# Kernel optimization log

Measured on AMD Instinct MI355X. Metric: run time of the kernel, lower is better.

The kernel has to match this reference:

```python
import jax, jax.numpy as jnp
import numpy as np

N = 100_000      # nodes
E = 1_600_000    # edges (avg degree 16)
D = 64           # node feature dim
C = 2            # num_classes
K = 2            # propagation hops


def setup_inputs() -> dict:
    key = jax.random.key(0)
    k1, k2, k3 = jax.random.split(key, 3)
    x = jax.random.normal(k1, (N, D), dtype=jnp.float32)
    edge_index = jax.random.randint(k2, (2, E), 0, N, dtype=jnp.int64)
    W = jax.random.normal(k3, (C, D), dtype=jnp.float32) * 0.1  # torch Linear weight [out,in]
    b = jnp.zeros((C,), dtype=jnp.float32)
    return {"x": x, "edge_index": edge_index, "W": W, "b": b}


def reference(x, edge_index, W, b):
    n = x.shape[0]
    self_loop = jnp.arange(n, dtype=edge_index.dtype)
    row = jnp.concatenate([edge_index[0], self_loop])  # source
    col = jnp.concatenate([edge_index[1], self_loop])  # target
    # GCN symmetric normalization with self-loops (PyG gcn_norm)
    deg = jax.ops.segment_sum(jnp.ones(col.shape, dtype=x.dtype), col, num_segments=n)
    dinv = jnp.where(deg > 0, jax.lax.rsqrt(deg), 0.0)
    norm = dinv[row] * dinv[col]                      # [E+N]
    # K-hop propagation: x <- A_hat x
    for _ in range(K):
        x = jax.ops.segment_sum(norm[:, None] * x[row], col, num_segments=n)
    logits = x @ W.T + b                               # [N, C]
    return jax.nn.log_softmax(logits, axis=1)
```

## Files before the change

kernel.cpp:

```cpp
#include <hip/hip_runtime.h>
#include <hip/hip_bf16.h>
#include <math.h>


#define NODES 100000
#define EDGES 1600000
#define DIM 64

#define PBITS 8
#define PSIZE 256
#define P_BUCKETS 391
#define CAP 8192

#define PART_BLOCKS 128
#define PART_PAIRS (EDGES / 2 / PART_BLOCKS)

#define PROJ_BLOCKS 782
#define NODES_PER_PROJ 128
#define K1_BLOCKS (PART_BLOCKS + PROJ_BLOCKS)

__global__ __launch_bounds__(256) void partproj_kernel(
    const void* __restrict__ ei, int* __restrict__ cursor,
    int* __restrict__ ecbuf, const float* __restrict__ x,
    const float* __restrict__ W, float4* __restrict__ uq) {
  const int t = threadIdx.x;
  if (blockIdx.x < PART_BLOCKS) {
    __shared__ int shMode;
    __shared__ int lcnt[P_BUCKETS];
    __shared__ int lbase[P_BUCKETS];
    if (t < 64) {
      const int* p = (const int*)ei;
      unsigned long long ball = __ballot(p[2 * t + 1] == 0);
      if (t == 0) shMode = (ball == ~0ULL) ? 1 : 0;
    }
    for (int i = t; i < P_BUCKETS; i += 256) lcnt[i] = 0;
    __syncthreads();
    const int m = shMode;
    const int pbase = blockIdx.x * PART_PAIRS;

    if (m) {
      const longlong2* cp =
          (const longlong2*)((const long long*)ei + EDGES) + pbase;
      for (int i = t; i < PART_PAIRS; i += 256) {
        longlong2 v = cp[i];
        atomicAdd(&lcnt[((int)v.x) >> PBITS], 1);
        atomicAdd(&lcnt[((int)v.y) >> PBITS], 1);
      }
    } else {
      const int2* cp = (const int2*)((const int*)ei + EDGES) + pbase;
      for (int i = t; i < PART_PAIRS; i += 256) {
        int2 v = cp[i];
        atomicAdd(&lcnt[v.x >> PBITS], 1);
        atomicAdd(&lcnt[v.y >> PBITS], 1);
      }
    }
    __syncthreads();
    for (int i = t; i < P_BUCKETS; i += 256) {
      int c = lcnt[i];
      lbase[i] = c ? atomicAdd(&cursor[i], c) : 0;
      lcnt[i] = 0;
    }
    __syncthreads();

    if (m) {
      const longlong2* rp = (const longlong2*)ei + pbase;
      const longlong2* cp =
          (const longlong2*)((const long long*)ei + EDGES) + pbase;
      for (int i = t; i < PART_PAIRS; i += 256) {
        longlong2 rv = rp[i];
        longlong2 cv = cp[i];
        {
          int r = (int)rv.x, c = (int)cv.x, bk = c >> PBITS;
          int rel = lbase[bk] + atomicAdd(&lcnt[bk], 1);
          if (rel < CAP)
            ecbuf[bk * CAP + rel] = (r << PBITS) | (c & (PSIZE - 1));
        }
        {
          int r = (int)rv.y, c = (int)cv.y, bk = c >> PBITS;
          int rel = lbase[bk] + atomicAdd(&lcnt[bk], 1);
          if (rel < CAP)
            ecbuf[bk * CAP + rel] = (r << PBITS) | (c & (PSIZE - 1));
        }
      }
    } else {
      const int2* rp = (const int2*)ei + pbase;
      const int2* cp = (const int2*)((const int*)ei + EDGES) + pbase;
      for (int i = t; i < PART_PAIRS; i += 256) {
        int2 rv = rp[i];
        int2 cv = cp[i];
        {
          int bk = cv.x >> PBITS;
          int rel = lbase[bk] + atomicAdd(&lcnt[bk], 1);
          if (rel < CAP)
            ecbuf[bk * CAP + rel] = (rv.x << PBITS) | (cv.x & (PSIZE - 1));
        }
        {
          int bk = cv.y >> PBITS;
          int rel = lbase[bk] + atomicAdd(&lcnt[bk], 1);
          if (rel < CAP)
            ecbuf[bk * CAP + rel] = (rv.y << PBITS) | (cv.y & (PSIZE - 1));
        }
      }
    }
  } else {
    const int nbase = (blockIdx.x - PART_BLOCKS) * NODES_PER_PROJ;
    const int lane16 = t & 15;
    const int sub = t >> 4;
    const float4 w0 = *(const float4*)&W[lane16 * 4];
    const float4 w1 = *(const float4*)&W[DIM + lane16 * 4];
    for (int k = sub; k < NODES_PER_PROJ; k += 16) {
      const int node = nbase + k;
      if (node < NODES) {
        float4 xv = *(const float4*)&x[(size_t)node * DIM + lane16 * 4];
        float p0 = xv.x * w0.x + xv.y * w0.y + xv.z * w0.z + xv.w * w0.w;
        float p1 = xv.x * w1.x + xv.y * w1.y + xv.z * w1.z + xv.w * w1.w;
#pragma unroll
        for (int off = 8; off >= 1; off >>= 1) {
          p0 += __shfl_xor(p0, off, 16);
          p1 += __shfl_xor(p1, off, 16);
        }
        if (lane16 == 0) *(float2*)&uq[node] = make_float2(p0, p1);
      }
    }
  }
}

__global__ __launch_bounds__(1024) void deg_kernel(
    const int* __restrict__ cursor, const int* __restrict__ ecbuf,
    float4* __restrict__ uq) {
  __shared__ int h[PSIZE];
  const int b = blockIdx.x;
  const int t = threadIdx.x;
  if (t < PSIZE) h[t] = 0;
  __syncthreads();
  const int cnt = min(cursor[b], CAP);
  const int4* ep4 = (const int4*)(ecbuf + b * CAP);
  for (int i = t; 4 * i < cnt; i += 1024) {
    int4 v = ep4[i];
    int base = 4 * i;
    if (base + 0 < cnt) atomicAdd(&h[v.x & (PSIZE - 1)], 1);
    if (base + 1 < cnt) atomicAdd(&h[v.y & (PSIZE - 1)], 1);
    if (base + 2 < cnt) atomicAdd(&h[v.z & (PSIZE - 1)], 1);
    if (base + 3 < cnt) atomicAdd(&h[v.w & (PSIZE - 1)], 1);
  }
  __syncthreads();
  if (t < PSIZE) {
    const int node = (b << PBITS) + t;
    if (node < NODES) uq[node].z = rsqrtf((float)(h[t] + 1));
  }
}

__global__ __launch_bounds__(1024) void hop1_kernel(
    const int* __restrict__ cursor, const int* __restrict__ ecbuf,
    const float4* __restrict__ uq, float2* __restrict__ z) {
  __shared__ float ax[PSIZE];
  __shared__ float ay[PSIZE];
  const int b = blockIdx.x;
  const int t = threadIdx.x;
  if (t < PSIZE) {
    ax[t] = 0.f;
    ay[t] = 0.f;
  }
  __syncthreads();
  const int cnt = min(cursor[b], CAP);
  const int4* ep4 = (const int4*)(ecbuf + b * CAP);
  for (int i = t; 4 * i < cnt; i += 1024) {
    int4 v = ep4[i];
    int base = 4 * i;
#pragma unroll
    for (int k = 0; k < 4; k++) {
      int pk = (k == 0) ? v.x : (k == 1) ? v.y : (k == 2) ? v.z : v.w;
      if (base + k < cnt) {
        float4 q = uq[pk >> PBITS];
        int l = pk & (PSIZE - 1);
        atomicAdd(&ax[l], q.z * q.x);
        atomicAdd(&ay[l], q.z * q.y);
      }
    }
  }
  __syncthreads();
  if (t < PSIZE) {
    const int node = (b << PBITS) + t;
    if (node < NODES) {
      float4 q = uq[node];
      float d = q.z;
      float s = d * d;
      z[node] = make_float2(s * (ax[t] + d * q.x), s * (ay[t] + d * q.y));
    }
  }
}

__global__ __launch_bounds__(1024) void hop2_kernel(
    const int* __restrict__ cursor, const int* __restrict__ ecbuf,
    const float2* __restrict__ z, const float4* __restrict__ uq,
    const float* __restrict__ bias, float2* __restrict__ out) {
  __shared__ float ax[PSIZE];
  __shared__ float ay[PSIZE];
  const int b = blockIdx.x;
  const int t = threadIdx.x;
  if (t < PSIZE) {
    ax[t] = 0.f;
    ay[t] = 0.f;
  }
  __syncthreads();
  const int cnt = min(cursor[b], CAP);
  const int4* ep4 = (const int4*)(ecbuf + b * CAP);
  for (int i = t; 4 * i < cnt; i += 1024) {
    int4 v = ep4[i];
    int base = 4 * i;
#pragma unroll
    for (int k = 0; k < 4; k++) {
      int pk = (k == 0) ? v.x : (k == 1) ? v.y : (k == 2) ? v.z : v.w;
      if (base + k < cnt) {
        float2 zv = z[pk >> PBITS];
        int l = pk & (PSIZE - 1);
        atomicAdd(&ax[l], zv.x);
        atomicAdd(&ay[l], zv.y);
      }
    }
  }
  __syncthreads();
  if (t < PSIZE) {
    const int node = (b << PBITS) + t;
    if (node < NODES) {
      float d = uq[node].z;
      float2 zi = z[node];
      float l0 = d * (ax[t] + zi.x) + bias[0];
      float l1 = d * (ay[t] + zi.y) + bias[1];
      float m = fmaxf(l0, l1);
      float ls = m + logf(expf(l0 - m) + expf(l1 - m));
      out[node] = make_float2(l0 - ls, l1 - ls);
    }
  }
}

extern "C" void kernel_launch(void* const* d_in, const int* in_sizes, int n_in,
                              void* d_out, int out_size, void* d_ws,
                              size_t ws_size, hipStream_t stream) {
  const float* x = (const float*)d_in[0];
  const void* ei = d_in[1];
  const float* W = (const float*)d_in[2];
  const float* bias = (const float*)d_in[3];
  float2* out = (float2*)d_out;

  char* w = (char*)d_ws;
  size_t off = 0;
  auto alloc = [&](size_t bytes) -> char* {
    char* p = w + off;
    off += (bytes + 255) & ~(size_t)255;
    return p;
  };
  int* cursor = (int*)alloc(P_BUCKETS * sizeof(int));
  int* ecbuf = (int*)alloc((size_t)P_BUCKETS * CAP * sizeof(int));
  float4* uq = (float4*)alloc((size_t)(P_BUCKETS << PBITS) * sizeof(float4));
  float2* z = (float2*)alloc((size_t)NODES * sizeof(float2));
  (void)ws_size;

  hipMemsetAsync(cursor, 0, P_BUCKETS * sizeof(int), stream);
  partproj_kernel<<<K1_BLOCKS, 256, 0, stream>>>(ei, cursor, ecbuf, x, W, uq);
  deg_kernel<<<P_BUCKETS, 1024, 0, stream>>>(cursor, ecbuf, uq);
  hop1_kernel<<<P_BUCKETS, 1024, 0, stream>>>(cursor, ecbuf, uq, z);
  hop2_kernel<<<P_BUCKETS, 1024, 0, stream>>>(cursor, ecbuf, z, uq, bias, out);
}
```

Before: 159.5 us.

## Halve bucket size, retune partition blocks, and split node data into packed arrays

Shrinks node buckets from 256 to 128 nodes, so there are 782 buckets each handled by a 256-thread block, and raises the partition grid to 625 blocks of 512 threads. It also replaces the float4 per-node record with separate float2 and float arrays. The degree kernel now precomputes d*u, so hop1 gathers 8 bytes per edge instead of 16. The goal is more parallel blocks, smaller per-block working sets, and less gather traffic, at the cost of more global cursor atomics, a tighter CAP margin per bucket (3072 for about 2048 expected edges), and extra writes in the degree kernel.

Measured after the change: 165.8 us. 3.9% more time.

```diff
diff --git a/kernel.cpp b/kernel.cpp
--- a/kernel.cpp
+++ b/kernel.cpp
@@ -7,22 +7,22 @@
 #define EDGES 1600000
 #define DIM 64
 
-#define PBITS 8
-#define PSIZE 256
-#define P_BUCKETS 391
-#define CAP 8192
-
-#define PART_BLOCKS 128
+#define PBITS 7
+#define PSIZE 128
+#define P_BUCKETS 782
+#define CAP 3072
+
+#define PART_BLOCKS 625
 #define PART_PAIRS (EDGES / 2 / PART_BLOCKS)
 
 #define PROJ_BLOCKS 782
 #define NODES_PER_PROJ 128
 #define K1_BLOCKS (PART_BLOCKS + PROJ_BLOCKS)
 
-__global__ __launch_bounds__(256) void partproj_kernel(
+__global__ __launch_bounds__(512) void partproj_kernel(
     const void* __restrict__ ei, int* __restrict__ cursor,
     int* __restrict__ ecbuf, const float* __restrict__ x,
-    const float* __restrict__ W, float4* __restrict__ uq) {
+    const float* __restrict__ W, float2* __restrict__ u) {
   const int t = threadIdx.x;
   if (blockIdx.x < PART_BLOCKS) {
     __shared__ int shMode;
@@ -33,7 +33,7 @@
       unsigned long long ball = __ballot(p[2 * t + 1] == 0);
       if (t == 0) shMode = (ball == ~0ULL) ? 1 : 0;
     }
-    for (int i = t; i < P_BUCKETS; i += 256) lcnt[i] = 0;
+    for (int i = t; i < P_BUCKETS; i += 512) lcnt[i] = 0;
     __syncthreads();
     const int m = shMode;
     const int pbase = blockIdx.x * PART_PAIRS;
@@ -41,21 +41,21 @@
     if (m) {
       const longlong2* cp =
           (const longlong2*)((const long long*)ei + EDGES) + pbase;
-      for (int i = t; i < PART_PAIRS; i += 256) {
+      for (int i = t; i < PART_PAIRS; i += 512) {
         longlong2 v = cp[i];
         atomicAdd(&lcnt[((int)v.x) >> PBITS], 1);
         atomicAdd(&lcnt[((int)v.y) >> PBITS], 1);
       }
     } else {
       const int2* cp = (const int2*)((const int*)ei + EDGES) + pbase;
-      for (int i = t; i < PART_PAIRS; i += 256) {
+      for (int i = t; i < PART_PAIRS; i += 512) {
         int2 v = cp[i];
         atomicAdd(&lcnt[v.x >> PBITS], 1);
         atomicAdd(&lcnt[v.y >> PBITS], 1);
       }
     }
     __syncthreads();
-    for (int i = t; i < P_BUCKETS; i += 256) {
+    for (int i = t; i < P_BUCKETS; i += 512) {
       int c = lcnt[i];
       lbase[i] = c ? atomicAdd(&cursor[i], c) : 0;
       lcnt[i] = 0;
@@ -66,7 +66,7 @@
       const longlong2* rp = (const longlong2*)ei + pbase;
       const longlong2* cp =
           (const longlong2*)((const long long*)ei + EDGES) + pbase;
-      for (int i = t; i < PART_PAIRS; i += 256) {
+      for (int i = t; i < PART_PAIRS; i += 512) {
         longlong2 rv = rp[i];
         longlong2 cv = cp[i];
         {
@@ -85,7 +85,7 @@
     } else {
       const int2* rp = (const int2*)ei + pbase;
       const int2* cp = (const int2*)((const int*)ei + EDGES) + pbase;
-      for (int i = t; i < PART_PAIRS; i += 256) {
+      for (int i = t; i < PART_PAIRS; i += 512) {
         int2 rv = rp[i];
         int2 cv = cp[i];
         {
@@ -108,7 +108,7 @@
     const int sub = t >> 4;
     const float4 w0 = *(const float4*)&W[lane16 * 4];
     const float4 w1 = *(const float4*)&W[DIM + lane16 * 4];
-    for (int k = sub; k < NODES_PER_PROJ; k += 16) {
+    for (int k = sub; k < NODES_PER_PROJ; k += 32) {
       const int node = nbase + k;
       if (node < NODES) {
         float4 xv = *(const float4*)&x[(size_t)node * DIM + lane16 * 4];
@@ -119,15 +119,16 @@
           p0 += __shfl_xor(p0, off, 16);
           p1 += __shfl_xor(p1, off, 16);
         }
-        if (lane16 == 0) *(float2*)&uq[node] = make_float2(p0, p1);
-      }
-    }
-  }
-}
-
-__global__ __launch_bounds__(1024) void deg_kernel(
+        if (lane16 == 0) u[node] = make_float2(p0, p1);
+      }
+    }
+  }
+}
+
+__global__ __launch_bounds__(256) void deg_kernel(
     const int* __restrict__ cursor, const int* __restrict__ ecbuf,
-    float4* __restrict__ uq) {
+    const float2* __restrict__ u, float2* __restrict__ v2,
+    float* __restrict__ dv) {
   __shared__ int h[PSIZE];
   const int b = blockIdx.x;
   const int t = threadIdx.x;
@@ -135,7 +136,7 @@
   __syncthreads();
   const int cnt = min(cursor[b], CAP);
   const int4* ep4 = (const int4*)(ecbuf + b * CAP);
-  for (int i = t; 4 * i < cnt; i += 1024) {
+  for (int i = t; 4 * i < cnt; i += 256) {
     int4 v = ep4[i];
     int base = 4 * i;
     if (base + 0 < cnt) atomicAdd(&h[v.x & (PSIZE - 1)], 1);
@@ -146,13 +147,19 @@
   __syncthreads();
   if (t < PSIZE) {
     const int node = (b << PBITS) + t;
-    if (node < NODES) uq[node].z = rsqrtf((float)(h[t] + 1));
-  }
-}
-
-__global__ __launch_bounds__(1024) void hop1_kernel(
+    if (node < NODES) {
+      float d = rsqrtf((float)(h[t] + 1));
+      float2 uu = u[node];
+      dv[node] = d;
+      v2[node] = make_float2(d * uu.x, d * uu.y);
+    }
+  }
+}
+
+__global__ __launch_bounds__(256) void hop1_kernel(
     const int* __restrict__ cursor, const int* __restrict__ ecbuf,
-    const float4* __restrict__ uq, float2* __restrict__ z) {
+    const float2* __restrict__ v2, const float* __restrict__ dv,
+    float2* __restrict__ z) {
   __shared__ float ax[PSIZE];
   __shared__ float ay[PSIZE];
   const int b = blockIdx.x;
@@ -164,17 +171,17 @@
   __syncthreads();
   const int cnt = min(cursor[b], CAP);
   const int4* ep4 = (const int4*)(ecbuf + b * CAP);
-  for (int i = t; 4 * i < cnt; i += 1024) {
+  for (int i = t; 4 * i < cnt; i += 256) {
     int4 v = ep4[i];
     int base = 4 * i;
 #pragma unroll
     for (int k = 0; k < 4; k++) {
       int pk = (k == 0) ? v.x : (k == 1) ? v.y : (k == 2) ? v.z : v.w;
       if (base + k < cnt) {
-        float4 q = uq[pk >> PBITS];
+        float2 s = v2[pk >> PBITS];
         int l = pk & (PSIZE - 1);
-        atomicAdd(&ax[l], q.z * q.x);
-        atomicAdd(&ay[l], q.z * q.y);
+        atomicAdd(&ax[l], s.x);
+        atomicAdd(&ay[l], s.y);
       }
     }
   }
@@ -182,17 +189,17 @@
   if (t < PSIZE) {
     const int node = (b << PBITS) + t;
     if (node < NODES) {
-      float4 q = uq[node];
-      float d = q.z;
-      float s = d * d;
-      z[node] = make_float2(s * (ax[t] + d * q.x), s * (ay[t] + d * q.y));
-    }
-  }
-}
-
-__global__ __launch_bounds__(1024) void hop2_kernel(
+      float d = dv[node];
+      float sc = d * d;
+      float2 vs = v2[node];
+      z[node] = make_float2(sc * (ax[t] + vs.x), sc * (ay[t] + vs.y));
+    }
+  }
+}
+
+__global__ __launch_bounds__(256) void hop2_kernel(
     const int* __restrict__ cursor, const int* __restrict__ ecbuf,
-    const float2* __restrict__ z, const float4* __restrict__ uq,
+    const float2* __restrict__ z, const float* __restrict__ dv,
     const float* __restrict__ bias, float2* __restrict__ out) {
   __shared__ float ax[PSIZE];
   __shared__ float ay[PSIZE];
@@ -205,7 +212,7 @@
   __syncthreads();
   const int cnt = min(cursor[b], CAP);
   const int4* ep4 = (const int4*)(ecbuf + b * CAP);
-  for (int i = t; 4 * i < cnt; i += 1024) {
+  for (int i = t; 4 * i < cnt; i += 256) {
     int4 v = ep4[i];
     int base = 4 * i;
 #pragma unroll
@@ -223,7 +230,7 @@
   if (t < PSIZE) {
     const int node = (b << PBITS) + t;
     if (node < NODES) {
-      float d = uq[node].z;
+      float d = dv[node];
       float2 zi = z[node];
       float l0 = d * (ax[t] + zi.x) + bias[0];
       float l1 = d * (ay[t] + zi.y) + bias[1];
@@ -250,15 +257,18 @@
     off += (bytes + 255) & ~(size_t)255;
     return p;
   };
+  const int NPAD = P_BUCKETS << PBITS;
   int* cursor = (int*)alloc(P_BUCKETS * sizeof(int));
   int* ecbuf = (int*)alloc((size_t)P_BUCKETS * CAP * sizeof(int));
-  float4* uq = (float4*)alloc((size_t)(P_BUCKETS << PBITS) * sizeof(float4));
-  float2* z = (float2*)alloc((size_t)NODES * sizeof(float2));
+  float2* u = (float2*)alloc((size_t)NPAD * sizeof(float2));
+  float2* v2 = (float2*)alloc((size_t)NPAD * sizeof(float2));
+  float* dv = (float*)alloc((size_t)NPAD * sizeof(float));
+  float2* z = (float2*)alloc((size_t)NPAD * sizeof(float2));
   (void)ws_size;
 
   hipMemsetAsync(cursor, 0, P_BUCKETS * sizeof(int), stream);
-  partproj_kernel<<<K1_BLOCKS, 256, 0, stream>>>(ei, cursor, ecbuf, x, W, uq);
-  deg_kernel<<<P_BUCKETS, 1024, 0, stream>>>(cursor, ecbuf, uq);
-  hop1_kernel<<<P_BUCKETS, 1024, 0, stream>>>(cursor, ecbuf, uq, z);
-  hop2_kernel<<<P_BUCKETS, 1024, 0, stream>>>(cursor, ecbuf, z, uq, bias, out);
-}
+  partproj_kernel<<<K1_BLOCKS, 512, 0, stream>>>(ei, cursor, ecbuf, x, W, u);
+  deg_kernel<<<P_BUCKETS, 256, 0, stream>>>(cursor, ecbuf, u, v2, dv);
+  hop1_kernel<<<P_BUCKETS, 256, 0, stream>>>(cursor, ecbuf, v2, dv, z);
+  hop2_kernel<<<P_BUCKETS, 256, 0, stream>>>(cursor, ecbuf, z, dv, bias, out);
+}
```
